# Performance work log

Hardware: AMD Instinct MI355X
Metric: run time of the kernel (lower is better)

The kernel has to match this reference:

```python
import jax, jax.numpy as jnp
import numpy as np

N_NODES = 16384
N_EDGES = 524288
N_GRAPHS = 256
IN_CH = 128
H_CH = 128   # per-head channels
HEADS = 2
LAYER_DIM = HEADS * H_CH  # 256, concat=True
POOL_DIM = 3 * LAYER_DIM  # 768
OUT_CH = 1
NEG_SLOPE = 0.2


def setup_inputs() -> dict:
    key = jax.random.key(0)
    ks = jax.random.split(key, 20)
    s = lambda k, shape, fan: jax.random.normal(k, shape, jnp.float32) * (1.0 / np.sqrt(fan))
    inp = {
        "x": jax.random.normal(ks[0], (N_NODES, IN_CH), jnp.float32),
        "edge_index": jax.random.randint(ks[1], (2, N_EDGES), 0, N_NODES, jnp.int64),
        "batch": jnp.sort(jax.random.randint(ks[2], (N_NODES,), 0, N_GRAPHS, jnp.int64)),
        # GATv2 layer 1 (in=128)
        "Wl1": s(ks[3], (IN_CH, LAYER_DIM), IN_CH), "Wr1": s(ks[4], (IN_CH, LAYER_DIM), IN_CH),
        "att1": s(ks[5], (HEADS, H_CH), H_CH), "b1": jnp.zeros((LAYER_DIM,), jnp.float32),
        # GATv2 layer 2 (in=256)
        "Wl2": s(ks[6], (LAYER_DIM, LAYER_DIM), LAYER_DIM), "Wr2": s(ks[7], (LAYER_DIM, LAYER_DIM), LAYER_DIM),
        "att2": s(ks[8], (HEADS, H_CH), H_CH), "b2": jnp.zeros((LAYER_DIM,), jnp.float32),
        # GATv2 layer 3 (in=256)
        "Wl3": s(ks[9], (LAYER_DIM, LAYER_DIM), LAYER_DIM), "Wr3": s(ks[10], (LAYER_DIM, LAYER_DIM), LAYER_DIM),
        "att3": s(ks[11], (HEADS, H_CH), H_CH), "b3": jnp.zeros((LAYER_DIM,), jnp.float32),
        # FFN (dropout inactive at eval)
        "fW1": s(ks[12], (POOL_DIM, POOL_DIM), POOL_DIM), "fb1": jnp.zeros((POOL_DIM,), jnp.float32),
        "fW2": s(ks[13], (POOL_DIM, OUT_CH), POOL_DIM), "fb2": jnp.zeros((OUT_CH,), jnp.float32),
    }
    return inp


def _gatv2(x, src, dst, Wl, Wr, att, b):
    """PyG GATv2Conv: per-edge score a . LeakyReLU(Wl x_src + Wr x_dst),
    softmax over incoming edges per destination, weighted scatter-add of Wl x_src."""
    n = x.shape[0]
    xl = (x @ Wl).reshape(n, HEADS, H_CH)  # source messages
    xr = (x @ Wr).reshape(n, HEADS, H_CH)  # target query
    e = jax.nn.leaky_relu(xl[src] + xr[dst], NEG_SLOPE)          # [E,H,C]
    logits = jnp.einsum('ehc,hc->eh', e, att)                    # [E,H]
    m = jax.ops.segment_max(logits, dst, num_segments=n)         # per-dst max (self-loops guarantee nonempty)
    ev = jnp.exp(logits - m[dst])
    denom = jax.ops.segment_sum(ev, dst, num_segments=n)
    alpha = ev / denom[dst]                                       # [E,H]
    out = jax.ops.segment_sum(alpha[..., None] * xl[src], dst, num_segments=n)  # [N,H,C]
    return out.reshape(n, LAYER_DIM) + b


def reference(x, edge_index, batch, Wl1, Wr1, att1, b1, Wl2, Wr2, att2, b2,
              Wl3, Wr3, att3, b3, fW1, fb1, fW2, fb2):
    n = x.shape[0]
    loops = jnp.arange(n, dtype=edge_index.dtype)
    src = jnp.concatenate([edge_index[0], loops])  # add_self_loops=True default
    dst = jnp.concatenate([edge_index[1], loops])
    h1 = _gatv2(x, src, dst, Wl1, Wr1, att1, b1)
    h2 = _gatv2(h1, src, dst, Wl2, Wr2, att2, b2)
    h3 = _gatv2(h2, src, dst, Wl3, Wr3, att3, b3)
    pool = lambda h: jax.ops.segment_sum(h, batch, num_segments=N_GRAPHS)
    h = jnp.concatenate([pool(h1), pool(h2), pool(h3)], axis=1)   # [G,768]
    h = jax.nn.relu(h @ fW1 + fb1)
    return h @ fW2 + fb2                                           # [G,1]
```

## Files before the change

kernel.cpp:

```cpp
#include <hip/hip_runtime.h>

#define NNODES 16384
#define NEDGES 524288
#define NETOT  (NEDGES + NNODES)
#define NGRAPH 256

typedef __attribute__((ext_vector_type(8))) short short8;
typedef __attribute__((ext_vector_type(4))) float f32x4;
typedef __attribute__((ext_vector_type(2))) float f32x2;
typedef __attribute__((ext_vector_type(4))) unsigned int u32x4;

__device__ __forceinline__ float b2f(unsigned short u){
  union { unsigned int i; float f; } v; v.i = ((unsigned int)u) << 16; return v.f;
}
__device__ __forceinline__ unsigned short f2b(float f){
  union { float f; unsigned int i; } v; v.f = f;
  unsigned int r = v.i + 0x7FFFu + ((v.i >> 16) & 1u);
  return (unsigned short)(r >> 16);
}
__device__ __forceinline__ f32x2 unpack2(unsigned int u){
  union { unsigned int i; float f; } lo, hi;
  lo.i = u << 16; hi.i = u & 0xFFFF0000u;
  f32x2 r; r[0] = lo.f; r[1] = hi.f; return r;
}

__global__ void __launch_bounds__(256) zero_deg(int* __restrict__ deg){
  deg[blockIdx.x * 256 + threadIdx.x] = 0;
}

__global__ void __launch_bounds__(256) count_deg(const int* __restrict__ ei, int* __restrict__ deg){
  int i = blockIdx.x * 256 + threadIdx.x;
  int d = (i < NEDGES) ? ei[NEDGES + i] : (i - NEDGES);
  atomicAdd(&deg[d], 1);
}

__global__ void __launch_bounds__(256) scan1(const int* __restrict__ deg,
                                             int* __restrict__ incl, int* __restrict__ bsum){
  __shared__ int ws[4];
  const int b = blockIdx.x, t = threadIdx.x, lane = t & 63, w = t >> 6;
  int v = deg[b * 256 + t];
  int x = v;
  #pragma unroll
  for(int o = 1; o < 64; o <<= 1){ int u = __shfl_up(x, o, 64); if(lane >= o) x += u; }
  if(lane == 63) ws[w] = x;
  __syncthreads();
  int add = 0;
  #pragma unroll
  for(int j = 0; j < 4; j++) if(j < w) add += ws[j];
  incl[b * 256 + t] = x + add;
  if(t == 255) bsum[b] = x + add;
}

__global__ void __launch_bounds__(256) scan3(const int* __restrict__ deg, const int* __restrict__ incl,
                                             const int* __restrict__ bsum,
                                             int* __restrict__ row_off, int* __restrict__ cursor){
  __shared__ int boff_s;
  const int b = blockIdx.x, t = threadIdx.x;
  if(t < 64){
    int v = (t < b) ? bsum[t] : 0;
    #pragma unroll
    for(int o = 32; o > 0; o >>= 1) v += __shfl_xor(v, o, 64);
    if(t == 0) boff_s = v;
  }
  __syncthreads();
  const int i = b * 256 + t;
  int inc = incl[i] + boff_s;
  row_off[i + 1] = inc;
  cursor[i] = inc - deg[i];
  if(i == 0) row_off[0] = 0;
}

__global__ void __launch_bounds__(256) fill_csr(const int* __restrict__ ei, int* __restrict__ cursor,
                                                int* __restrict__ col_src){
  int i = blockIdx.x * 256 + threadIdx.x;
  int s, d;
  if(i < NEDGES){ s = ei[i]; d = ei[NEDGES + i]; }
  else          { s = i - NEDGES; d = s; }
  int p = atomicAdd(&cursor[d], 1);
  col_src[p] = s;
}

__global__ void __launch_bounds__(256) prep(const float* __restrict__ x,
                                            const float* __restrict__ Wl1, const float* __restrict__ Wr1,
                                            const float* __restrict__ Wl2, const float* __restrict__ Wr2,
                                            const float* __restrict__ Wl3, const float* __restrict__ Wr3,
                                            unsigned short* __restrict__ xb,
                                            unsigned short* __restrict__ Wt1,
                                            unsigned short* __restrict__ Wt2,
                                            unsigned short* __restrict__ Wt3){
  const int b = blockIdx.x, t = threadIdx.x;
  if(b < 8192){
    int i = b * 256 + t;
    xb[i] = f2b(x[i]);
    return;
  }
  const float *Wl, *Wr; unsigned short* Wt; int K, i;
  if(b < 8192 + 256){ Wl = Wl1; Wr = Wr1; Wt = Wt1; K = 128; i = (b - 8192) * 256 + t; }
  else if(b < 8192 + 256 + 512){ Wl = Wl2; Wr = Wr2; Wt = Wt2; K = 256; i = (b - 8448) * 256 + t; }
  else { Wl = Wl3; Wr = Wr3; Wt = Wt3; K = 256; i = (b - 8960) * 256 + t; }
  int k = i >> 9, c = i & 511;
  float val = (c < 256) ? Wl[(size_t)k * 256 + c] : Wr[(size_t)k * 256 + (c - 256)];
  Wt[(size_t)c * K + k] = f2b(val);
}

template<int K>
__global__ void __launch_bounds__(256) gemm_xw(const unsigned short* __restrict__ A,
                                               const unsigned short* __restrict__ Wt,
                                               unsigned short* __restrict__ Cout){
  __shared__ unsigned short As[128 * 32];
  __shared__ unsigned short Bs[128 * 32];
  const int t = threadIdx.x;
  const int rowbase = blockIdx.x * 128;
  const int colbase = blockIdx.y * 128;
  const int wave = t >> 6, lane = t & 63;
  const int lrow = lane & 15, kg = lane >> 4;

  f32x4 acc[2][8] = {};

  for(int kt = 0; kt < K; kt += 32){
    #pragma unroll
    for(int j = 0; j < 2; j++){
      const int ci  = (j * 4 + wave) * 64 + lane;
      const int row = ci >> 2, cst = ci & 3;
      const int c   = cst ^ ((row >> 1) & 3);
      const unsigned short* ga = A  + (size_t)(rowbase + row) * K + kt + c * 8;
      const unsigned short* gb = Wt + (size_t)(colbase + row) * K + kt + c * 8;
      __builtin_amdgcn_global_load_lds(
        (const __attribute__((address_space(1))) unsigned int*)ga,
        (__attribute__((address_space(3))) unsigned int*)(As + (j * 4 + wave) * 512),
        16, 0, 0);
      __builtin_amdgcn_global_load_lds(
        (const __attribute__((address_space(1))) unsigned int*)gb,
        (__attribute__((address_space(3))) unsigned int*)(Bs + (j * 4 + wave) * 512),
        16, 0, 0);
    }
    __syncthreads();

    short8 afrag[2], bfrag[8];
    #pragma unroll
    for(int rf = 0; rf < 2; rf++){
      int ra = wave * 32 + rf * 16 + lrow;
      int ca = kg ^ ((ra >> 1) & 3);
      afrag[rf] = *(const short8*)(As + ra * 32 + ca * 8);
    }
    #pragma unroll
    for(int fc = 0; fc < 8; fc++){
      int rb = fc * 16 + lrow;
      int cb = kg ^ ((rb >> 1) & 3);
      bfrag[fc] = *(const short8*)(Bs + rb * 32 + cb * 8);
    }
    #pragma unroll
    for(int rf = 0; rf < 2; rf++)
      #pragma unroll
      for(int fc = 0; fc < 8; fc++)
        acc[rf][fc] = __builtin_amdgcn_mfma_f32_16x16x32_bf16(afrag[rf], bfrag[fc], acc[rf][fc], 0, 0, 0);
    __syncthreads();
  }
  #pragma unroll
  for(int rf = 0; rf < 2; rf++)
    #pragma unroll
    for(int fc = 0; fc < 8; fc++)
      #pragma unroll
      for(int r = 0; r < 4; r++){
        int row = rowbase + wave * 32 + rf * 16 + kg * 4 + r;
        int col = colbase + fc * 16 + lrow;
        Cout[(size_t)row * 512 + col] = f2b(acc[rf][fc][r]);
      }
}

__global__ void __launch_bounds__(256) edge_agg(const unsigned short* __restrict__ xlb,
                                                const int* __restrict__ row_off,
                                                const int* __restrict__ col_src,
                                                const float* __restrict__ att,
                                                const float* __restrict__ bias,
                                                unsigned short* __restrict__ hout){
  const int n = (blockIdx.x * 256 + threadIdx.x) >> 6;
  const int lane = threadIdx.x & 63;
  const int eg = lane >> 4;
  const int c0 = (lane & 15) * 16;
  f32x2 xr[8], at[8];
  {
    const unsigned short* xp = xlb + (size_t)n * 512 + 256 + c0;
    u32x4 v0 = *(const u32x4*)xp;
    u32x4 v1 = *(const u32x4*)(xp + 8);
    xr[0] = unpack2(v0.x); xr[1] = unpack2(v0.y); xr[2] = unpack2(v0.z); xr[3] = unpack2(v0.w);
    xr[4] = unpack2(v1.x); xr[5] = unpack2(v1.y); xr[6] = unpack2(v1.z); xr[7] = unpack2(v1.w);
    #pragma unroll
    for(int i = 0; i < 8; i++) at[i] = *(const f32x2*)(att + c0 + 2 * i);
  }
  float s = 0.f;
  f32x2 ac[8] = {};
  const int beg = row_off[n], end = row_off[n + 1];
  for(int ch = beg; ch < end; ch += 64){
    int idx = ch + lane;
    int si = (idx < end) ? col_src[idx] : 0;
    int cnt = end - ch; if(cnt > 64) cnt = 64;
    int src0 = __shfl(si, eg);
    const unsigned short* gp0 = xlb + (size_t)src0 * 512 + c0;
    u32x4 va = *(const u32x4*)gp0;
    u32x4 vb = *(const u32x4*)(gp0 + 8);
    for(int k = 0; k < cnt; k += 4){
      int nk = k + 4 + eg; nk = (nk > 63) ? 63 : nk;
      int nsrc = __shfl(si, nk);
      const unsigned short* gpn = xlb + (size_t)nsrc * 512 + c0;
      u32x4 na = *(const u32x4*)gpn;
      u32x4 nb = *(const u32x4*)(gpn + 8);
      f32x2 x0 = unpack2(va.x), x1 = unpack2(va.y), x2 = unpack2(va.z), x3 = unpack2(va.w);
      f32x2 x4 = unpack2(vb.x), x5 = unpack2(vb.y), x6 = unpack2(vb.z), x7 = unpack2(vb.w);
      f32x2 e, p2;
      e = x0 + xr[0]; e = __builtin_elementwise_max(e, e * 0.2f); p2  = e * at[0];
      e = x1 + xr[1]; e = __builtin_elementwise_max(e, e * 0.2f); p2 += e * at[1];
      e = x2 + xr[2]; e = __builtin_elementwise_max(e, e * 0.2f); p2 += e * at[2];
      e = x3 + xr[3]; e = __builtin_elementwise_max(e, e * 0.2f); p2 += e * at[3];
      e = x4 + xr[4]; e = __builtin_elementwise_max(e, e * 0.2f); p2 += e * at[4];
      e = x5 + xr[5]; e = __builtin_elementwise_max(e, e * 0.2f); p2 += e * at[5];
      e = x6 + xr[6]; e = __builtin_elementwise_max(e, e * 0.2f); p2 += e * at[6];
      e = x7 + xr[7]; e = __builtin_elementwise_max(e, e * 0.2f); p2 += e * at[7];
      float p = p2[0] + p2[1];
      p += __shfl_xor(p, 1); p += __shfl_xor(p, 2); p += __shfl_xor(p, 4);
      float pe = (k + eg < cnt) ? __expf(p) : 0.f;
      s += pe;
      f32x2 pe2 = {pe, pe};
      ac[0] += pe2 * x0; ac[1] += pe2 * x1; ac[2] += pe2 * x2; ac[3] += pe2 * x3;
      ac[4] += pe2 * x4; ac[5] += pe2 * x5; ac[6] += pe2 * x6; ac[7] += pe2 * x7;
      va = na; vb = nb;
    }
  }
  s += __shfl_xor(s, 16); s += __shfl_xor(s, 32);
  #pragma unroll
  for(int i = 0; i < 8; i++){
    ac[i][0] += __shfl_xor(ac[i][0], 16); ac[i][0] += __shfl_xor(ac[i][0], 32);
    ac[i][1] += __shfl_xor(ac[i][1], 16); ac[i][1] += __shfl_xor(ac[i][1], 32);
  }
  if(eg == 0){
    float inv = 1.f / s;
    unsigned short o[16];
    #pragma unroll
    for(int i = 0; i < 8; i++){
      o[2 * i]     = f2b(fmaf(ac[i][0], inv, bias[c0 + 2 * i]));
      o[2 * i + 1] = f2b(fmaf(ac[i][1], inv, bias[c0 + 2 * i + 1]));
    }
    unsigned short* hp = hout + (size_t)n * 256 + c0;
    *(u32x4*)hp       = *(const u32x4*)&o[0];
    *(u32x4*)(hp + 8) = *(const u32x4*)&o[8];
  }
}

__device__ __forceinline__ int lbound(const int* __restrict__ a, int n, int v){
  int lo = 0, hi = n;
  while(lo < hi){ int mid = (lo + hi) >> 1; if(a[mid] < v) lo = mid + 1; else hi = mid; }
  return lo;
}

__global__ void __launch_bounds__(256) pool_accum(const unsigned short* __restrict__ h,
                                                  const int* __restrict__ batch,
                                                  float* __restrict__ pool, int slot){
  __shared__ float red[8][264];
  const int g = blockIdx.x, t = threadIdx.x;
  const int ng = t >> 5, c0 = (t & 31) * 8;
  const int lo = lbound(batch, NNODES, g);
  const int hi = lbound(batch, NNODES, g + 1);
  f32x2 a0 = {0.f,0.f}, a1 = {0.f,0.f}, a2 = {0.f,0.f}, a3 = {0.f,0.f};
  for(int node = lo + ng; node < hi; node += 8){
    u32x4 v = *(const u32x4*)(h + (size_t)node * 256 + c0);
    a0 += unpack2(v.x); a1 += unpack2(v.y); a2 += unpack2(v.z); a3 += unpack2(v.w);
  }
  red[ng][c0 + 0] = a0[0]; red[ng][c0 + 1] = a0[1];
  red[ng][c0 + 2] = a1[0]; red[ng][c0 + 3] = a1[1];
  red[ng][c0 + 4] = a2[0]; red[ng][c0 + 5] = a2[1];
  red[ng][c0 + 6] = a3[0]; red[ng][c0 + 7] = a3[1];
  __syncthreads();
  float s = 0.f;
  #pragma unroll
  for(int i = 0; i < 8; i++) s += red[i][t];
  pool[(size_t)g * 768 + slot * 256 + t] = s;
}

__global__ void __launch_bounds__(256) ffn1(const float* __restrict__ pool,
                                            const float* __restrict__ fW1,
                                            const float* __restrict__ fb1,
                                            float* __restrict__ hidden){
  __shared__ float ap[32][65];
  __shared__ float ws[64][33];
  const int t = threadIdx.x;
  const int cb = blockIdx.x * 32;
  const int gb = blockIdx.y * 32;
  const int tc = t & 31, tg = t >> 5;
  float acc[4] = {};
  for(int kc = 0; kc < 768; kc += 64){
    {
      int g_l = t >> 3, j8 = (t & 7) * 8;
      const float* gp = pool + (size_t)(gb + g_l) * 768 + kc + j8;
      #pragma unroll
      for(int i = 0; i < 8; i++) ap[g_l][j8 + i] = gp[i];
    }
    {
      int c_l = t & 31, k0 = (t >> 5) * 8;
      #pragma unroll
      for(int i = 0; i < 8; i++) ws[k0 + i][c_l] = fW1[(size_t)(kc + k0 + i) * 768 + cb + c_l];
    }
    __syncthreads();
    #pragma unroll
    for(int k = 0; k < 64; k++){
      float w = ws[k][tc];
      #pragma unroll
      for(int i = 0; i < 4; i++) acc[i] = fmaf(ap[tg * 4 + i][k], w, acc[i]);
    }
    __syncthreads();
  }
  float b = fb1[cb + tc];
  #pragma unroll
  for(int i = 0; i < 4; i++)
    hidden[(size_t)(gb + tg * 4 + i) * 768 + cb + tc] = fmaxf(acc[i] + b, 0.f);
}

__global__ void __launch_bounds__(256) ffn2(const float* __restrict__ hidden,
                                            const float* __restrict__ fW2,
                                            const float* __restrict__ fb2,
                                            float* __restrict__ out){
  const int g = (blockIdx.x * 256 + threadIdx.x) >> 6;
  const int lane = threadIdx.x & 63;
  float p = 0.f;
  for(int i = lane; i < 768; i += 64) p += hidden[(size_t)g * 768 + i] * fW2[i];
  #pragma unroll
  for(int o = 32; o > 0; o >>= 1) p += __shfl_xor(p, o, 64);
  if(lane == 0) out[g] = p + fb2[0];
}

extern "C" void kernel_launch(void* const* d_in, const int* in_sizes, int n_in,
                              void* d_out, int out_size, void* d_ws, size_t ws_size,
                              hipStream_t stream){
  const float* x    = (const float*)d_in[0];
  const int* ei     = (const int*)d_in[1];
  const int* batch  = (const int*)d_in[2];
  const float* Wl[3]  = {(const float*)d_in[3],  (const float*)d_in[7],  (const float*)d_in[11]};
  const float* Wr[3]  = {(const float*)d_in[4],  (const float*)d_in[8],  (const float*)d_in[12]};
  const float* att[3] = {(const float*)d_in[5],  (const float*)d_in[9],  (const float*)d_in[13]};
  const float* bp[3]  = {(const float*)d_in[6],  (const float*)d_in[10], (const float*)d_in[14]};
  const float* fW1 = (const float*)d_in[15];
  const float* fb1 = (const float*)d_in[16];
  const float* fW2 = (const float*)d_in[17];
  const float* fb2 = (const float*)d_in[18];

  char* ws = (char*)d_ws;
  size_t off = 0;
  auto alloc = [&](size_t sz){ size_t p = off; off += (sz + 255) & ~(size_t)255; return p; };
  int* deg      = (int*)(ws + alloc((size_t)NNODES * 4));
  int* rowoff   = (int*)(ws + alloc((size_t)(NNODES + 1) * 4));
  int* cursor   = (int*)(ws + alloc((size_t)NNODES * 4));
  int* colsrc   = (int*)(ws + alloc((size_t)NETOT * 4));
  int* incl     = (int*)(ws + alloc((size_t)NNODES * 4));
  int* bsum     = (int*)(ws + alloc(64 * 4));
  unsigned short* xb  = (unsigned short*)(ws + alloc((size_t)NNODES * 128 * 2));
  unsigned short* Wt1 = (unsigned short*)(ws + alloc((size_t)512 * 128 * 2));
  unsigned short* Wt2 = (unsigned short*)(ws + alloc((size_t)512 * 256 * 2));
  unsigned short* Wt3 = (unsigned short*)(ws + alloc((size_t)512 * 256 * 2));
  unsigned short* xlb = (unsigned short*)(ws + alloc((size_t)NNODES * 512 * 2));
  unsigned short* hA  = (unsigned short*)(ws + alloc((size_t)NNODES * 256 * 2));
  unsigned short* hB  = (unsigned short*)(ws + alloc((size_t)NNODES * 256 * 2));
  float* pool   = (float*)(ws + alloc((size_t)NGRAPH * 768 * 4));
  float* hidden = (float*)(ws + alloc((size_t)NGRAPH * 768 * 4));

  zero_deg<<<NNODES / 256, 256, 0, stream>>>(deg);
  count_deg<<<NETOT / 256, 256, 0, stream>>>(ei, deg);
  prep<<<8192 + 256 + 512 + 512, 256, 0, stream>>>(x, Wl[0], Wr[0], Wl[1], Wr[1], Wl[2], Wr[2],
                                                   xb, Wt1, Wt2, Wt3);
  scan1<<<NNODES / 256, 256, 0, stream>>>(deg, incl, bsum);
  scan3<<<NNODES / 256, 256, 0, stream>>>(deg, incl, bsum, rowoff, cursor);
  fill_csr<<<NETOT / 256, 256, 0, stream>>>(ei, cursor, colsrc);

  dim3 ggrid(NNODES / 128, 4);
  const int EAG = NNODES / 4;

  unsigned short* hbuf[3] = {hA, hB, hA};
  const unsigned short* abuf[3] = {xb, hA, hB};
  unsigned short* wbuf[3] = {Wt1, Wt2, Wt3};

  for(int L = 0; L < 3; L++){
    if(L == 0) gemm_xw<128><<<ggrid, 256, 0, stream>>>(abuf[0], wbuf[0], xlb);
    else       gemm_xw<256><<<ggrid, 256, 0, stream>>>(abuf[L], wbuf[L], xlb);
    edge_agg<<<EAG, 256, 0, stream>>>(xlb, rowoff, colsrc, att[L], bp[L], hbuf[L]);
    pool_accum<<<NGRAPH, 256, 0, stream>>>(hbuf[L], batch, pool, L);
  }

  ffn1<<<dim3(768 / 32, NGRAPH / 32), 256, 0, stream>>>(pool, fW1, fb1, hidden);
  ffn2<<<NGRAPH / 4, 256, 0, stream>>>(hidden, fW2, fb2, (float*)d_out);
}
```

Baseline: 277.4 us.

## Split edge aggregation across two waves, double-buffer GEMM, merge small kernels

The edge aggregation kernel now assigns two waves per destination node, each handling alternating groups of four edges, and combines partial sums and softmax denominators through LDS. The software prefetch of the next source row is removed. The GEMM gains double-buffered LDS staging so the next K-tile load overlaps the MFMAs, which also drops one barrier per iteration. Degree zeroing is folded into the prep kernel, and the three per-layer pooling launches become a single pool3 launch using a third h buffer. Together these aim to raise memory-level parallelism in the gather-heavy aggregation and cut launch count, at the cost of more LDS, an extra block barrier, and extra workspace.

```diff
diff --git a/kernel.cpp b/kernel.cpp
--- a/kernel.cpp
+++ b/kernel.cpp
@@ -22,10 +22,6 @@
   union { unsigned int i; float f; } lo, hi;
   lo.i = u << 16; hi.i = u & 0xFFFF0000u;
   f32x2 r; r[0] = lo.f; r[1] = hi.f; return r;
-}
-
-__global__ void __launch_bounds__(256) zero_deg(int* __restrict__ deg){
-  deg[blockIdx.x * 256 + threadIdx.x] = 0;
 }
 
 __global__ void __launch_bounds__(256) count_deg(const int* __restrict__ ei, int* __restrict__ deg){
@@ -87,11 +83,16 @@
                                             unsigned short* __restrict__ xb,
                                             unsigned short* __restrict__ Wt1,
                                             unsigned short* __restrict__ Wt2,
-                                            unsigned short* __restrict__ Wt3){
+                                            unsigned short* __restrict__ Wt3,
+                                            int* __restrict__ deg){
   const int b = blockIdx.x, t = threadIdx.x;
   if(b < 8192){
     int i = b * 256 + t;
     xb[i] = f2b(x[i]);
+    return;
+  }
+  if(b >= 9472){
+    deg[(b - 9472) * 256 + t] = 0;
     return;
   }
   const float *Wl, *Wr; unsigned short* Wt; int K, i;
@@ -107,8 +108,8 @@
 __global__ void __launch_bounds__(256) gemm_xw(const unsigned short* __restrict__ A,
                                                const unsigned short* __restrict__ Wt,
                                                unsigned short* __restrict__ Cout){
-  __shared__ unsigned short As[128 * 32];
-  __shared__ unsigned short Bs[128 * 32];
+  __shared__ unsigned short As[2][128 * 32];
+  __shared__ unsigned short Bs[2][128 * 32];
   const int t = threadIdx.x;
   const int rowbase = blockIdx.x * 128;
   const int colbase = blockIdx.y * 128;
@@ -117,7 +118,7 @@
 
   f32x4 acc[2][8] = {};
 
-  for(int kt = 0; kt < K; kt += 32){
+  auto stage = [&](int kt, int buf){
     #pragma unroll
     for(int j = 0; j < 2; j++){
       const int ci  = (j * 4 + wave) * 64 + lane;
@@ -127,34 +128,38 @@
       const unsigned short* gb = Wt + (size_t)(colbase + row) * K + kt + c * 8;
       __builtin_amdgcn_global_load_lds(
         (const __attribute__((address_space(1))) unsigned int*)ga,
-        (__attribute__((address_space(3))) unsigned int*)(As + (j * 4 + wave) * 512),
+        (__attribute__((address_space(3))) unsigned int*)(As[buf] + (j * 4 + wave) * 512),
         16, 0, 0);
       __builtin_amdgcn_global_load_lds(
         (const __attribute__((address_space(1))) unsigned int*)gb,
-        (__attribute__((address_space(3))) unsigned int*)(Bs + (j * 4 + wave) * 512),
+        (__attribute__((address_space(3))) unsigned int*)(Bs[buf] + (j * 4 + wave) * 512),
         16, 0, 0);
     }
+  };
+
+  stage(0, 0);
+  for(int kt = 0, it = 0; kt < K; kt += 32, it++){
+    const int cur = it & 1;
     __syncthreads();
-
     short8 afrag[2], bfrag[8];
     #pragma unroll
     for(int rf = 0; rf < 2; rf++){
       int ra = wave * 32 + rf * 16 + lrow;
       int ca = kg ^ ((ra >> 1) & 3);
-      afrag[rf] = *(const short8*)(As + ra * 32 + ca * 8);
+      afrag[rf] = *(const short8*)(As[cur] + ra * 32 + ca * 8);
     }
     #pragma unroll
     for(int fc = 0; fc < 8; fc++){
       int rb = fc * 16 + lrow;
       int cb = kg ^ ((rb >> 1) & 3);
-      bfrag[fc] = *(const short8*)(Bs + rb * 32 + cb * 8);
-    }
+      bfrag[fc] = *(const short8*)(Bs[cur] + rb * 32 + cb * 8);
+    }
+    if(kt + 32 < K) stage(kt + 32, cur ^ 1);
     #pragma unroll
     for(int rf = 0; rf < 2; rf++)
       #pragma unroll
       for(int fc = 0; fc < 8; fc++)
         acc[rf][fc] = __builtin_amdgcn_mfma_f32_16x16x32_bf16(afrag[rf], bfrag[fc], acc[rf][fc], 0, 0, 0);
-    __syncthreads();
   }
   #pragma unroll
   for(int rf = 0; rf < 2; rf++)
@@ -174,7 +179,11 @@
                                                 const float* __restrict__ att,
                                                 const float* __restrict__ bias,
                                                 unsigned short* __restrict__ hout){
-  const int n = (blockIdx.x * 256 + threadIdx.x) >> 6;
+  __shared__ float acbuf[4][256];
+  __shared__ float sbuf[4][2];
+  const int w = threadIdx.x >> 6;
+  const int n = blockIdx.x * 2 + (w >> 1);
+  const int half = w & 1;
   const int lane = threadIdx.x & 63;
   const int eg = lane >> 4;
   const int c0 = (lane & 15) * 16;
@@ -195,18 +204,14 @@
     int idx = ch + lane;
     int si = (idx < end) ? col_src[idx] : 0;
     int cnt = end - ch; if(cnt > 64) cnt = 64;
-    int src0 = __shfl(si, eg);
-    const unsigned short* gp0 = xlb + (size_t)src0 * 512 + c0;
-    u32x4 va = *(const u32x4*)gp0;
-    u32x4 vb = *(const u32x4*)(gp0 + 8);
-    for(int k = 0; k < cnt; k += 4){
-      int nk = k + 4 + eg; nk = (nk > 63) ? 63 : nk;
-      int nsrc = __shfl(si, nk);
-      const unsigned short* gpn = xlb + (size_t)nsrc * 512 + c0;
-      u32x4 na = *(const u32x4*)gpn;
-      u32x4 nb = *(const u32x4*)(gpn + 8);
-      f32x2 x0 = unpack2(va.x), x1 = unpack2(va.y), x2 = unpack2(va.z), x3 = unpack2(va.w);
-      f32x2 x4 = unpack2(vb.x), x5 = unpack2(vb.y), x6 = unpack2(vb.z), x7 = unpack2(vb.w);
+    for(int k = half * 4; k < cnt; k += 8){
+      int kk = k + eg;
+      int src = __shfl(si, kk);
+      const unsigned short* gp = xlb + (size_t)src * 512 + c0;
+      u32x4 v0 = *(const u32x4*)gp;
+      u32x4 v1 = *(const u32x4*)(gp + 8);
+      f32x2 x0 = unpack2(v0.x), x1 = unpack2(v0.y), x2 = unpack2(v0.z), x3 = unpack2(v0.w);
+      f32x2 x4 = unpack2(v1.x), x5 = unpack2(v1.y), x6 = unpack2(v1.z), x7 = unpack2(v1.w);
       f32x2 e, p2;
       e = x0 + xr[0]; e = __builtin_elementwise_max(e, e * 0.2f); p2  = e * at[0];
       e = x1 + xr[1]; e = __builtin_elementwise_max(e, e * 0.2f); p2 += e * at[1];
@@ -218,12 +223,11 @@
       e = x7 + xr[7]; e = __builtin_elementwise_max(e, e * 0.2f); p2 += e * at[7];
       float p = p2[0] + p2[1];
       p += __shfl_xor(p, 1); p += __shfl_xor(p, 2); p += __shfl_xor(p, 4);
-      float pe = (k + eg < cnt) ? __expf(p) : 0.f;
+      float pe = (kk < cnt) ? __expf(p) : 0.f;
       s += pe;
       f32x2 pe2 = {pe, pe};
       ac[0] += pe2 * x0; ac[1] += pe2 * x1; ac[2] += pe2 * x2; ac[3] += pe2 * x3;
       ac[4] += pe2 * x4; ac[5] += pe2 * x5; ac[6] += pe2 * x6; ac[7] += pe2 * x7;
-      va = na; vb = nb;
     }
   }
   s += __shfl_xor(s, 16); s += __shfl_xor(s, 32);
@@ -233,12 +237,23 @@
     ac[i][1] += __shfl_xor(ac[i][1], 16); ac[i][1] += __shfl_xor(ac[i][1], 32);
   }
   if(eg == 0){
-    float inv = 1.f / s;
+    #pragma unroll
+    for(int i = 0; i < 8; i++){
+      acbuf[w][c0 + 2 * i]     = ac[i][0];
+      acbuf[w][c0 + 2 * i + 1] = ac[i][1];
+    }
+    if(lane == 0) sbuf[w][0] = s;
+    if(lane == 8) sbuf[w][1] = s;
+  }
+  __syncthreads();
+  if(half == 0 && eg == 0){
+    const int hh = lane >> 3;
+    float inv = 1.f / (sbuf[w][hh] + sbuf[w + 1][hh]);
     unsigned short o[16];
     #pragma unroll
-    for(int i = 0; i < 8; i++){
-      o[2 * i]     = f2b(fmaf(ac[i][0], inv, bias[c0 + 2 * i]));
-      o[2 * i + 1] = f2b(fmaf(ac[i][1], inv, bias[c0 + 2 * i + 1]));
+    for(int i = 0; i < 16; i++){
+      float v = acbuf[w][c0 + i] + acbuf[w + 1][c0 + i];
+      o[i] = f2b(fmaf(v, inv, bias[c0 + i]));
     }
     unsigned short* hp = hout + (size_t)n * 256 + c0;
     *(u32x4*)hp       = *(const u32x4*)&o[0];
@@ -252,11 +267,14 @@
   return lo;
 }
 
-__global__ void __launch_bounds__(256) pool_accum(const unsigned short* __restrict__ h,
-                                                  const int* __restrict__ batch,
-                                                  float* __restrict__ pool, int slot){
+__global__ void __launch_bounds__(256) pool3(const unsigned short* __restrict__ hA,
+                                             const unsigned short* __restrict__ hB,
+                                             const unsigned short* __restrict__ hC,
+                                             const int* __restrict__ batch,
+                                             float* __restrict__ pool){
   __shared__ float red[8][264];
-  const int g = blockIdx.x, t = threadIdx.x;
+  const int g = blockIdx.x, slot = blockIdx.y, t = threadIdx.x;
+  const unsigned short* h = (slot == 0) ? hA : ((slot == 1) ? hB : hC);
   const int ng = t >> 5, c0 = (t & 31) * 8;
   const int lo = lbound(batch, NNODES, g);
   const int hi = lbound(batch, NNODES, g + 1);
@@ -358,21 +376,21 @@
   unsigned short* xlb = (unsigned short*)(ws + alloc((size_t)NNODES * 512 * 2));
   unsigned short* hA  = (unsigned short*)(ws + alloc((size_t)NNODES * 256 * 2));
   unsigned short* hB  = (unsigned short*)(ws + alloc((size_t)NNODES * 256 * 2));
+  unsigned short* hC  = (unsigned short*)(ws + alloc((size_t)NNODES * 256 * 2));
   float* pool   = (float*)(ws + alloc((size_t)NGRAPH * 768 * 4));
   float* hidden = (float*)(ws + alloc((size_t)NGRAPH * 768 * 4));
 
-  zero_deg<<<NNODES / 256, 256, 0, stream>>>(deg);
+  prep<<<9536, 256, 0, stream>>>(x, Wl[0], Wr[0], Wl[1], Wr[1], Wl[2], Wr[2],
+                                 xb, Wt1, Wt2, Wt3, deg);
   count_deg<<<NETOT / 256, 256, 0, stream>>>(ei, deg);
-  prep<<<8192 + 256 + 512 + 512, 256, 0, stream>>>(x, Wl[0], Wr[0], Wl[1], Wr[1], Wl[2], Wr[2],
-                                                   xb, Wt1, Wt2, Wt3);
   scan1<<<NNODES / 256, 256, 0, stream>>>(deg, incl, bsum);
   scan3<<<NNODES / 256, 256, 0, stream>>>(deg, incl, bsum, rowoff, cursor);
   fill_csr<<<NETOT / 256, 256, 0, stream>>>(ei, cursor, colsrc);
 
   dim3 ggrid(NNODES / 128, 4);
-  const int EAG = NNODES / 4;
-
-  unsigned short* hbuf[3] = {hA, hB, hA};
+  const int EAG = NNODES / 2;
+
+  unsigned short* hbuf[3] = {hA, hB, hC};
   const unsigned short* abuf[3] = {xb, hA, hB};
   unsigned short* wbuf[3] = {Wt1, Wt2, Wt3};
 
@@ -380,9 +398,9 @@
     if(L == 0) gemm_xw<128><<<ggrid, 256, 0, stream>>>(abuf[0], wbuf[0], xlb);
     else       gemm_xw<256><<<ggrid, 256, 0, stream>>>(abuf[L], wbuf[L], xlb);
     edge_agg<<<EAG, 256, 0, stream>>>(xlb, rowoff, colsrc, att[L], bp[L], hbuf[L]);
-    pool_accum<<<NGRAPH, 256, 0, stream>>>(hbuf[L], batch, pool, L);
-  }
-
+  }
+
+  pool3<<<dim3(NGRAPH, 3), 256, 0, stream>>>(hA, hB, hC, batch, pool);
   ffn1<<<dim3(768 / 32, NGRAPH / 32), 256, 0, stream>>>(pool, fW1, fb1, hidden);
   ffn2<<<NGRAPH / 4, 256, 0, stream>>>(hidden, fW2, fb2, (float*)d_out);
 }
```

Result: no change. 279.2 us (+0.7%).
